# Kernel optimization log

Measured on AMD Instinct MI355X. Metric: run time of the kernel, lower is better.

## Reference

```python
import jax, jax.numpy as jnp
import numpy as np

N_HEADS = 16


def setup_inputs() -> dict:
    key = jax.random.key(0)
    k1, k2, k3, k4 = jax.random.split(key, 4)
    b, s, d = 2, 2048, 1024
    x = jax.random.normal(k1, (b, s, d), dtype=jnp.float32)
    attn_B = jax.random.normal(k2, (b, N_HEADS, s, s), dtype=jnp.float32) * 0.02
    W_attn = jax.random.normal(k3, (d, 3 * d), dtype=jnp.float32) * (1.0 / np.sqrt(d))
    b_attn = jax.random.normal(k4, (3 * d,), dtype=jnp.float32) * 0.01
    return {"x": x, "attn_B": attn_B, "W_attn": W_attn, "b_attn": b_attn}


def reference(x, attn_B, W_attn, b_attn):
    b, s, d = x.shape
    h = N_HEADS
    hd = d // h
    qkv = x @ W_attn + b_attn                       # [b, s, 3d]
    Q, K, V = jnp.split(qkv, 3, axis=-1)
    # [b, s, d] -> [b, h, s, hd]
    Q = Q.reshape(b, s, h, hd).transpose(0, 2, 1, 3)
    K = K.reshape(b, s, h, hd).transpose(0, 2, 1, 3)
    V = V.reshape(b, s, h, hd).transpose(0, 2, 1, 3)
    scale = 1.0 / jnp.sqrt(jnp.asarray(hd, dtype=Q.dtype))
    scores = jnp.einsum("bhqk,bhsk->bhqs", Q, K) * scale   # [b, h, s, s]
    attn = jax.nn.softmax(scores, axis=-1) + attn_B          # post-softmax additive bias
    y = jnp.einsum("bhqs,bhsd->bhqd", attn, V)               # [b, h, s, hd]
    y = y.transpose(0, 2, 1, 3).reshape(b, s, d)
    return y
```

## Files before the change

### kernel.cpp

```cpp
#include <hip/hip_runtime.h>
#include <hip/hip_bf16.h>


typedef __attribute__((ext_vector_type(4))) float  f32x4;
typedef __attribute__((ext_vector_type(8))) short  bf16x8;
typedef __attribute__((ext_vector_type(4))) short  s16x4;

__device__ __forceinline__ short f2bf(float f) {
    __hip_bfloat16 h = __float2bfloat16(f);
    return __builtin_bit_cast(short, h);
}

__device__ __forceinline__ void gll16(const short* g, short* l) {
    __builtin_amdgcn_global_load_lds(
        (const __attribute__((address_space(1))) void*)g,
        (__attribute__((address_space(3))) void*)l, 16, 0, 0);
}

__global__ void conv_x_kernel(const float* __restrict__ x, short* __restrict__ xb) {
    int idx = blockIdx.x * 256 + threadIdx.x;
    f32x4 v = *reinterpret_cast<const f32x4*>(x + (size_t)idx * 4);
    s16x4 o;
    o[0] = f2bf(v[0]); o[1] = f2bf(v[1]); o[2] = f2bf(v[2]); o[3] = f2bf(v[3]);
    *reinterpret_cast<s16x4*>(xb + (size_t)idx * 4) = o;
}

__global__ void wtrans_kernel(const float* __restrict__ W, short* __restrict__ Wt) {
    __shared__ float tile[64][65];
    int kb = blockIdx.x, nb = blockIdx.y;
    int t = threadIdx.x;
    int c4 = (t & 15) * 4;
    int r0 = t >> 4;
#pragma unroll
    for (int rr = 0; rr < 4; ++rr) {
        int kl = r0 + rr * 16;
        f32x4 v = *reinterpret_cast<const f32x4*>(W + (size_t)(kb * 64 + kl) * 3072 + nb * 64 + c4);
        tile[kl][c4 + 0] = v[0]; tile[kl][c4 + 1] = v[1];
        tile[kl][c4 + 2] = v[2]; tile[kl][c4 + 3] = v[3];
    }
    __syncthreads();
#pragma unroll
    for (int rr = 0; rr < 4; ++rr) {
        int nl = r0 + rr * 16;
        s16x4 o;
#pragma unroll
        for (int i = 0; i < 4; ++i) o[i] = f2bf(tile[c4 + i][nl]);
        *reinterpret_cast<s16x4*>(Wt + (size_t)(nb * 64 + nl) * 1024 + kb * 64 + c4) = o;
    }
}

__global__ __launch_bounds__(256) void qkv_gemm_kernel(
    const short* __restrict__ xb, const short* __restrict__ Wt,
    const float* __restrict__ bias,
    short* __restrict__ Qo, short* __restrict__ Ko, short* __restrict__ Vo)
{
    __shared__ short As[128 * 64];
    __shared__ short Bs[128 * 64];
    int tid = threadIdx.x;
    int wave = tid >> 6, lane = tid & 63, g = lane >> 4, lr = lane & 15;
    int wr = wave >> 1, wc = wave & 1;
    int bm = blockIdx.x, bn = blockIdx.y;

    f32x4 acc[4][4];
#pragma unroll
    for (int a = 0; a < 4; ++a)
#pragma unroll
        for (int b = 0; b < 4; ++b) acc[a][b] = (f32x4){0.f, 0.f, 0.f, 0.f};

    for (int k0 = 0; k0 < 1024; k0 += 64) {
#pragma unroll
        for (int j = 0; j < 4; ++j) {
            int c = j * 256 + tid;
            int row = c >> 3, cc = c & 7;
            int scc = (cc ^ (row & 7)) * 8;
            gll16(xb + (size_t)(bm * 128 + row) * 1024 + k0 + scc,
                  &As[(j * 256 + wave * 64) * 8]);
            gll16(Wt + (size_t)(bn * 128 + row) * 1024 + k0 + scc,
                  &Bs[(j * 256 + wave * 64) * 8]);
        }
        __syncthreads();

        bf16x8 af[2][4], bfr[2][4];
#pragma unroll
        for (int mt = 0; mt < 4; ++mt) {
            int row = wr * 64 + mt * 16 + lr;
            af[0][mt] = *reinterpret_cast<const bf16x8*>(&As[row * 64 + (((g    ) ^ (lr & 7)) * 8)]);
            af[1][mt] = *reinterpret_cast<const bf16x8*>(&As[row * 64 + (((g + 4) ^ (lr & 7)) * 8)]);
        }
#pragma unroll
        for (int nt = 0; nt < 4; ++nt) {
            int row = wc * 64 + nt * 16 + lr;
            bfr[0][nt] = *reinterpret_cast<const bf16x8*>(&Bs[row * 64 + (((g    ) ^ (lr & 7)) * 8)]);
            bfr[1][nt] = *reinterpret_cast<const bf16x8*>(&Bs[row * 64 + (((g + 4) ^ (lr & 7)) * 8)]);
        }
#pragma unroll
        for (int mt = 0; mt < 4; ++mt)
#pragma unroll
            for (int nt = 0; nt < 4; ++nt) {
                acc[mt][nt] = __builtin_amdgcn_mfma_f32_16x16x32_bf16(af[0][mt], bfr[0][nt], acc[mt][nt], 0, 0, 0);
                acc[mt][nt] = __builtin_amdgcn_mfma_f32_16x16x32_bf16(af[1][mt], bfr[1][nt], acc[mt][nt], 0, 0, 0);
            }
        __syncthreads();
    }

#pragma unroll
    for (int nt = 0; nt < 4; ++nt) {
        int n = bn * 128 + wc * 64 + nt * 16 + lr;
        float bv = bias[n];
        int which = n >> 10;
        int h = (n >> 6) & 15;
        int dd = n & 63;
        short* base = (which == 0) ? Qo : (which == 1) ? Ko : Vo;
#pragma unroll
        for (int mt = 0; mt < 4; ++mt) {
#pragma unroll
            for (int r = 0; r < 4; ++r) {
                int m = bm * 128 + wr * 64 + mt * 16 + g * 4 + r;
                int bb = m >> 11, s = m & 2047;
                float v = acc[mt][nt][r] + bv;
                base[(((size_t)bb * 16 + h) * 2048 + s) * 64 + dd] = f2bf(v);
            }
        }
    }
}

__global__ __launch_bounds__(256) void vtrans_kernel(const short* __restrict__ V, short* __restrict__ Vt) {
    __shared__ short t[64][72];
    int st = blockIdx.x, bh = blockIdx.y;
    int tid = threadIdx.x;
#pragma unroll
    for (int j = 0; j < 2; ++j) {
        int c = j * 256 + tid;
        int row = c >> 3, cc = c & 7;
        bf16x8 v = *reinterpret_cast<const bf16x8*>(V + (size_t)((bh * 2048) + st * 64 + row) * 64 + cc * 8);
        *reinterpret_cast<bf16x8*>(&t[row][cc * 8]) = v;
    }
    __syncthreads();
#pragma unroll
    for (int j = 0; j < 2; ++j) {
        int c = j * 256 + tid;
        int d = c >> 3, cs = c & 7;
        bf16x8 o;
#pragma unroll
        for (int i = 0; i < 8; ++i) o[i] = t[cs * 8 + i][d];
        *reinterpret_cast<bf16x8*>(Vt + (size_t)(bh * 64 + d) * 2048 + st * 64 + cs * 8) = o;
    }
}

__global__ __launch_bounds__(256) void attn_kernel(
    const short* __restrict__ Qw, const short* __restrict__ Kw, const short* __restrict__ Vtw,
    const float* __restrict__ attnB, float* __restrict__ out)
{
    __shared__ short Ks [2][64 * 64];
    __shared__ short Vts[2][64 * 64];
    __shared__ short Ps [4][16 * 64];

    int qt = blockIdx.x, bh = blockIdx.y;
    int b = bh >> 4, h = bh & 15;
    int tid = threadIdx.x;
    int wave = tid >> 6, lane = tid & 63, g = lane >> 4, lr = lane & 15;

    const short* Qb = Qw  + (size_t)bh * 2048 * 64;
    const short* Kb = Kw  + (size_t)bh * 2048 * 64;
    const short* Vb = Vtw + (size_t)bh * 64 * 2048;
    const float* Bp = attnB + (size_t)bh * 2048 * 2048;

    int qbase = qt * 64 + wave * 16;

    bf16x8 qf0, qf1;
    {
        const short* qp = Qb + (size_t)(qbase + lr) * 64 + g * 8;
        qf0 = *reinterpret_cast<const bf16x8*>(qp);
        qf1 = *reinterpret_cast<const bf16x8*>(qp + 32);
    }
    const float* brow = Bp + (size_t)(qbase + lr) * 2048 + g * 8;

    f32x4 Os[4], Ob[4];
#pragma unroll
    for (int dt = 0; dt < 4; ++dt) { Os[dt] = (f32x4){0.f,0.f,0.f,0.f}; Ob[dt] = (f32x4){0.f,0.f,0.f,0.f}; }
    float lpart[4] = {0.f, 0.f, 0.f, 0.f};

#define STAGE_KV(buf, ktt) do {                                                   \
    _Pragma("unroll")                                                             \
    for (int j = 0; j < 2; ++j) {                                                 \
        int c = j * 256 + tid;                                                    \
        int row = c >> 3, cc = c & 7;                                             \
        int scc = (cc ^ (row & 7)) * 8;                                           \
        gll16(Kb + (size_t)((ktt) * 64 + row) * 64 + scc,                         \
              &Ks[buf][(j * 256 + wave * 64) * 8]);                               \
        gll16(Vb + (size_t)row * 2048 + (ktt) * 64 + scc,                         \
              &Vts[buf][(j * 256 + wave * 64) * 8]);                              \
    }                                                                             \
} while (0)

    STAGE_KV(0, 0);
    __syncthreads();

    for (int kt = 0; kt < 32; ++kt) {
        int cur = kt & 1;
        if (kt < 31) STAGE_KV(cur ^ 1, kt + 1);

        f32x4 bfl0 = *reinterpret_cast<const f32x4*>(brow + kt * 64);
        f32x4 bfl1 = *reinterpret_cast<const f32x4*>(brow + kt * 64 + 4);
        f32x4 bfl2 = *reinterpret_cast<const f32x4*>(brow + kt * 64 + 32);
        f32x4 bfl3 = *reinterpret_cast<const f32x4*>(brow + kt * 64 + 36);

        f32x4 S[4];
        __builtin_amdgcn_s_setprio(1);
#pragma unroll
        for (int nt = 0; nt < 4; ++nt) {
            int row = nt * 16 + lr;
            bf16x8 kf0 = *reinterpret_cast<const bf16x8*>(&Ks[cur][row * 64 + (((g    ) ^ (lr & 7)) * 8)]);
            bf16x8 kf1 = *reinterpret_cast<const bf16x8*>(&Ks[cur][row * 64 + (((g + 4) ^ (lr & 7)) * 8)]);
            f32x4 s = (f32x4){0.f,0.f,0.f,0.f};
            s = __builtin_amdgcn_mfma_f32_16x16x32_bf16(qf0, kf0, s, 0, 0, 0);
            s = __builtin_amdgcn_mfma_f32_16x16x32_bf16(qf1, kf1, s, 0, 0, 0);
            S[nt] = s;
        }
        __builtin_amdgcn_s_setprio(0);

#pragma unroll
        for (int nt = 0; nt < 4; ++nt)
#pragma unroll
            for (int r = 0; r < 4; ++r) {
                float p = __expf(S[nt][r] * 0.125f);
                S[nt][r] = p;
                lpart[r] += p;
            }

#pragma unroll
        for (int nt = 0; nt < 4; ++nt)
#pragma unroll
            for (int r = 0; r < 4; ++r) {
                int q = g * 4 + r;
                int col = nt * 16 + lr;
                Ps[wave][q * 64 + (((col >> 3) ^ (q & 7)) * 8) + (col & 7)] = f2bf(S[nt][r]);
            }

        bf16x8 bbf0, bbf1;
#pragma unroll
        for (int i = 0; i < 4; ++i) {
            bbf0[i]     = f2bf(bfl0[i]);
            bbf0[i + 4] = f2bf(bfl1[i]);
            bbf1[i]     = f2bf(bfl2[i]);
            bbf1[i + 4] = f2bf(bfl3[i]);
        }

        bf16x8 pf0 = *reinterpret_cast<const bf16x8*>(&Ps[wave][lr * 64 + (((g    ) ^ (lr & 7)) * 8)]);
        bf16x8 pf1 = *reinterpret_cast<const bf16x8*>(&Ps[wave][lr * 64 + (((g + 4) ^ (lr & 7)) * 8)]);

        __builtin_amdgcn_s_setprio(1);
#pragma unroll
        for (int dt = 0; dt < 4; ++dt) {
            int row = dt * 16 + lr;
            bf16x8 v0 = *reinterpret_cast<const bf16x8*>(&Vts[cur][row * 64 + (((g    ) ^ (lr & 7)) * 8)]);
            bf16x8 v1 = *reinterpret_cast<const bf16x8*>(&Vts[cur][row * 64 + (((g + 4) ^ (lr & 7)) * 8)]);
            Os[dt] = __builtin_amdgcn_mfma_f32_16x16x32_bf16(pf0,  v0, Os[dt], 0, 0, 0);
            Os[dt] = __builtin_amdgcn_mfma_f32_16x16x32_bf16(pf1,  v1, Os[dt], 0, 0, 0);
            Ob[dt] = __builtin_amdgcn_mfma_f32_16x16x32_bf16(bbf0, v0, Ob[dt], 0, 0, 0);
            Ob[dt] = __builtin_amdgcn_mfma_f32_16x16x32_bf16(bbf1, v1, Ob[dt], 0, 0, 0);
        }
        __builtin_amdgcn_s_setprio(0);

        __syncthreads();
    }
#undef STAGE_KV

#pragma unroll
    for (int r = 0; r < 4; ++r) {
        float l = lpart[r];
        l += __shfl_xor(l, 1);
        l += __shfl_xor(l, 2);
        l += __shfl_xor(l, 4);
        l += __shfl_xor(l, 8);
        float inv = 1.0f / l;
        int q = qbase + g * 4 + r;
#pragma unroll
        for (int dt = 0; dt < 4; ++dt) {
            int dcol = dt * 16 + lr;
            out[((size_t)(b * 2048 + q) * 16 + h) * 64 + dcol] = Os[dt][r] * inv + Ob[dt][r];
        }
    }
}

extern "C" void kernel_launch(void* const* d_in, const int* in_sizes, int n_in,
                              void* d_out, int out_size, void* d_ws, size_t ws_size,
                              hipStream_t stream) {
    const float* x     = (const float*)d_in[0];
    const float* attnB = (const float*)d_in[1];
    const float* W     = (const float*)d_in[2];
    const float* bias  = (const float*)d_in[3];
    float* out = (float*)d_out;

    short* ws = (short*)d_ws;
    short* xb = ws;
    short* Wt = xb + 4194304;
    short* Q  = Wt + 3145728;
    short* K  = Q  + 4194304;
    short* V  = K  + 4194304;
    short* Vt = V  + 4194304;

    conv_x_kernel<<<4096, 256, 0, stream>>>(x, xb);
    wtrans_kernel<<<dim3(16, 48), 256, 0, stream>>>(W, Wt);
    qkv_gemm_kernel<<<dim3(32, 24), 256, 0, stream>>>(xb, Wt, bias, Q, K, V);
    vtrans_kernel<<<dim3(32, 32), 256, 0, stream>>>(V, Vt);
    attn_kernel<<<dim3(32, 32), 256, 0, stream>>>(Q, K, Vt, attnB, out);
}
```

Before: 228.6 us.

## Prefetch bias one tile ahead, transpose QK MFMA, pack P stores with cvt_pk

The attention loop now prefetches the next tile's post-softmax bias into registers and swaps __syncthreads for a manual vmcnt wait plus s_barrier, so the bias load overlaps a full iteration. The QK^T MFMA operands are swapped, so each lane holds scores for one query row. That lets P be written to LDS as packed 32-bit bf16 pairs via v_cvt_pk_bf16_f32 and reduces the row-sum to a single per-lane accumulator. It also adds exp2 with a prescaled constant and a launch_bounds occupancy hint. The cost is more live registers and fragile hand-written waitcnt counting.

```diff
diff --git a/kernel.cpp b/kernel.cpp
--- a/kernel.cpp
+++ b/kernel.cpp
@@ -9,6 +9,12 @@
 __device__ __forceinline__ short f2bf(float f) {
     __hip_bfloat16 h = __float2bfloat16(f);
     return __builtin_bit_cast(short, h);
+}
+
+__device__ __forceinline__ unsigned cvt_pk_bf16(float lo, float hi) {
+    unsigned w;
+    asm("v_cvt_pk_bf16_f32 %0, %1, %2" : "=v"(w) : "v"(lo), "v"(hi));
+    return w;
 }
 
 __device__ __forceinline__ void gll16(const short* g, short* l) {
@@ -147,7 +153,7 @@
     }
 }
 
-__global__ __launch_bounds__(256) void attn_kernel(
+__global__ __launch_bounds__(256, 4) void attn_kernel(
     const short* __restrict__ Qw, const short* __restrict__ Kw, const short* __restrict__ Vtw,
     const float* __restrict__ attnB, float* __restrict__ out)
 {
@@ -178,7 +184,7 @@
     f32x4 Os[4], Ob[4];
 #pragma unroll
     for (int dt = 0; dt < 4; ++dt) { Os[dt] = (f32x4){0.f,0.f,0.f,0.f}; Ob[dt] = (f32x4){0.f,0.f,0.f,0.f}; }
-    float lpart[4] = {0.f, 0.f, 0.f, 0.f};
+    float lsum = 0.f;
 
 #define STAGE_KV(buf, ktt) do {                                                   \
     _Pragma("unroll")                                                             \
@@ -193,17 +199,38 @@
     }                                                                             \
 } while (0)
 
+    f32x4 bfn0, bfn1, bfn2, bfn3;
     STAGE_KV(0, 0);
-    __syncthreads();
+    __builtin_amdgcn_sched_barrier(0);
+    bfn0 = *reinterpret_cast<const f32x4*>(brow);
+    bfn1 = *reinterpret_cast<const f32x4*>(brow + 4);
+    bfn2 = *reinterpret_cast<const f32x4*>(brow + 32);
+    bfn3 = *reinterpret_cast<const f32x4*>(brow + 36);
+    asm volatile("s_waitcnt vmcnt(4)" ::: "memory");
+    __builtin_amdgcn_s_barrier();
+    __builtin_amdgcn_sched_barrier(0);
 
     for (int kt = 0; kt < 32; ++kt) {
         int cur = kt & 1;
-        if (kt < 31) STAGE_KV(cur ^ 1, kt + 1);
-
-        f32x4 bfl0 = *reinterpret_cast<const f32x4*>(brow + kt * 64);
-        f32x4 bfl1 = *reinterpret_cast<const f32x4*>(brow + kt * 64 + 4);
-        f32x4 bfl2 = *reinterpret_cast<const f32x4*>(brow + kt * 64 + 32);
-        f32x4 bfl3 = *reinterpret_cast<const f32x4*>(brow + kt * 64 + 36);
+
+        unsigned bb0 = cvt_pk_bf16(bfn0[0], bfn0[1]);
+        unsigned bb1 = cvt_pk_bf16(bfn0[2], bfn0[3]);
+        unsigned bb2 = cvt_pk_bf16(bfn1[0], bfn1[1]);
+        unsigned bb3 = cvt_pk_bf16(bfn1[2], bfn1[3]);
+        unsigned bb4 = cvt_pk_bf16(bfn2[0], bfn2[1]);
+        unsigned bb5 = cvt_pk_bf16(bfn2[2], bfn2[3]);
+        unsigned bb6 = cvt_pk_bf16(bfn3[0], bfn3[1]);
+        unsigned bb7 = cvt_pk_bf16(bfn3[2], bfn3[3]);
+
+        if (kt < 31) {
+            STAGE_KV(cur ^ 1, kt + 1);
+            __builtin_amdgcn_sched_barrier(0);
+            const float* bp = brow + (kt + 1) * 64;
+            bfn0 = *reinterpret_cast<const f32x4*>(bp);
+            bfn1 = *reinterpret_cast<const f32x4*>(bp + 4);
+            bfn2 = *reinterpret_cast<const f32x4*>(bp + 32);
+            bfn3 = *reinterpret_cast<const f32x4*>(bp + 36);
+        }
 
         f32x4 S[4];
         __builtin_amdgcn_s_setprio(1);
@@ -213,8 +240,8 @@
             bf16x8 kf0 = *reinterpret_cast<const bf16x8*>(&Ks[cur][row * 64 + (((g    ) ^ (lr & 7)) * 8)]);
             bf16x8 kf1 = *reinterpret_cast<const bf16x8*>(&Ks[cur][row * 64 + (((g + 4) ^ (lr & 7)) * 8)]);
             f32x4 s = (f32x4){0.f,0.f,0.f,0.f};
-            s = __builtin_amdgcn_mfma_f32_16x16x32_bf16(qf0, kf0, s, 0, 0, 0);
-            s = __builtin_amdgcn_mfma_f32_16x16x32_bf16(qf1, kf1, s, 0, 0, 0);
+            s = __builtin_amdgcn_mfma_f32_16x16x32_bf16(kf0, qf0, s, 0, 0, 0);
+            s = __builtin_amdgcn_mfma_f32_16x16x32_bf16(kf1, qf1, s, 0, 0, 0);
             S[nt] = s;
         }
         __builtin_amdgcn_s_setprio(0);
@@ -223,31 +250,32 @@
         for (int nt = 0; nt < 4; ++nt)
 #pragma unroll
             for (int r = 0; r < 4; ++r) {
-                float p = __expf(S[nt][r] * 0.125f);
+                float p = exp2f(S[nt][r] * 0.1803368801111f);
                 S[nt][r] = p;
-                lpart[r] += p;
+                lsum += p;
             }
 
+        short* psw = &Ps[wave][lr * 64];
 #pragma unroll
         for (int nt = 0; nt < 4; ++nt)
 #pragma unroll
-            for (int r = 0; r < 4; ++r) {
-                int q = g * 4 + r;
-                int col = nt * 16 + lr;
-                Ps[wave][q * 64 + (((col >> 3) ^ (q & 7)) * 8) + (col & 7)] = f2bf(S[nt][r]);
+            for (int rp = 0; rp < 2; ++rp) {
+                unsigned w = cvt_pk_bf16(S[nt][2 * rp], S[nt][2 * rp + 1]);
+                int kp = 8 * nt + 2 * g + rp;
+                int bi = kp >> 2, off = kp & 3;
+                *reinterpret_cast<unsigned*>(psw + ((bi ^ (lr & 7)) << 3) + off * 2) = w;
             }
-
-        bf16x8 bbf0, bbf1;
-#pragma unroll
-        for (int i = 0; i < 4; ++i) {
-            bbf0[i]     = f2bf(bfl0[i]);
-            bbf0[i + 4] = f2bf(bfl1[i]);
-            bbf1[i]     = f2bf(bfl2[i]);
-            bbf1[i + 4] = f2bf(bfl3[i]);
-        }
 
         bf16x8 pf0 = *reinterpret_cast<const bf16x8*>(&Ps[wave][lr * 64 + (((g    ) ^ (lr & 7)) * 8)]);
         bf16x8 pf1 = *reinterpret_cast<const bf16x8*>(&Ps[wave][lr * 64 + (((g + 4) ^ (lr & 7)) * 8)]);
+        bf16x8 bbf0, bbf1;
+        {
+            typedef __attribute__((ext_vector_type(4))) unsigned u32x4;
+            u32x4 t0 = (u32x4){bb0, bb1, bb2, bb3};
+            u32x4 t1 = (u32x4){bb4, bb5, bb6, bb7};
+            bbf0 = __builtin_bit_cast(bf16x8, t0);
+            bbf1 = __builtin_bit_cast(bf16x8, t1);
+        }
 
         __builtin_amdgcn_s_setprio(1);
 #pragma unroll
@@ -262,23 +290,26 @@
         }
         __builtin_amdgcn_s_setprio(0);
 
-        __syncthreads();
+        if (kt < 31) {
+            asm volatile("s_waitcnt vmcnt(4)" ::: "memory");
+            __builtin_amdgcn_s_barrier();
+            __builtin_amdgcn_sched_barrier(0);
+        }
     }
 #undef STAGE_KV
 
+    float l = lsum;
+    l += __shfl_xor(l, 16);
+    l += __shfl_xor(l, 32);
+    float inv = 1.0f / l;
 #pragma unroll
     for (int r = 0; r < 4; ++r) {
-        float l = lpart[r];
-        l += __shfl_xor(l, 1);
-        l += __shfl_xor(l, 2);
-        l += __shfl_xor(l, 4);
-        l += __shfl_xor(l, 8);
-        float inv = 1.0f / l;
+        float invr = __shfl(inv, g * 4 + r);
         int q = qbase + g * 4 + r;
 #pragma unroll
         for (int dt = 0; dt < 4; ++dt) {
             int dcol = dt * 16 + lr;
-            out[((size_t)(b * 2048 + q) * 16 + h) * 64 + dcol] = Os[dt][r] * inv + Ob[dt][r];
+            out[((size_t)(b * 2048 + q) * 16 + h) * 64 + dcol] = Os[dt][r] * invr + Ob[dt][r];
         }
     }
 }
```

Measured after the change: 206.6 us. 1.11x faster.
